# Performance work log

Hardware: AMD Instinct MI355X
Metric: run time of the kernel (lower is better)

## Reference

```python
import jax, jax.numpy as jnp
import numpy as np

DIM = 1024
HIDDEN = 4096
N_EXPERTS = 8
K = 2
TEMP = 1.0


def setup_inputs() -> dict:
    key = jax.random.key(0)
    ks = jax.random.split(key, 7)
    s = 0.02
    x = jax.random.normal(ks[0], (4, 2048, DIM), dtype=jnp.float32)
    router_w = jax.random.normal(ks[1], (N_EXPERTS, DIM), dtype=jnp.float32) * s
    router_b = jnp.zeros((N_EXPERTS,), dtype=jnp.float32)
    # Expert(dim, hidden, 'swiglu'): fc1: dim -> 2*hidden, fc2: hidden -> dim
    w1 = jax.random.normal(ks[2], (N_EXPERTS, 2 * HIDDEN, DIM), dtype=jnp.float32) * s
    b1 = jnp.zeros((N_EXPERTS, 2 * HIDDEN), dtype=jnp.float32)
    w2 = jax.random.normal(ks[3], (N_EXPERTS, DIM, HIDDEN), dtype=jnp.float32) * s
    b2 = jnp.zeros((N_EXPERTS, DIM), dtype=jnp.float32)
    return {"x": x, "router_w": router_w, "router_b": router_b,
            "w1": w1, "b1": b1, "w2": w2, "b2": b2}


def _expert_ffn(xf, wa, ba, wb, bb):
    # xf: [T, dim]; swiglu FFN
    h = xf @ wa.T + ba                       # [T, 2*hidden]
    h1, h2 = jnp.split(h, 2, axis=-1)
    h = jax.nn.silu(h1) * h2                 # [T, hidden]
    return h @ wb.T + bb                     # [T, dim]


def reference(x, router_w, router_b, w1, b1, w2, b2):
    b, t, d = x.shape
    logits = (x @ router_w.T + router_b) / TEMP          # [b, t, E]
    topk_val, topk_idx = jax.lax.top_k(logits, K)        # [b, t, K]
    weights = jax.nn.softmax(topk_val, axis=-1)          # [b, t, K]

    xf = x.reshape(-1, d)                                # [T, dim]
    # Compute every expert on all tokens (dense reference for irregular dispatch)
    outs = jax.vmap(_expert_ffn, in_axes=(None, 0, 0, 0, 0))(xf, w1, b1, w2, b2)  # [E, T, dim]
    outs = jnp.transpose(outs, (1, 0, 2))                # [T, E, dim]

    idx = topk_idx.reshape(-1, K)                        # [T, K]
    gathered = jnp.take_along_axis(outs, idx[:, :, None], axis=1)  # [T, K, dim]
    combined = (gathered * weights.reshape(-1, K, 1)).sum(axis=1)  # [T, dim]
    return combined.reshape(b, t, d)
```

## Files before the change

### kernel.cpp

```cpp
#include <hip/hip_runtime.h>

#define T_TOK 8192
#define DIMX 1024
#define HID 4096
#define NE 8
#define TP (T_TOK * 2)
#define PADR 128
#define BK 64

typedef unsigned short ushort_t;
typedef __attribute__((ext_vector_type(4))) float f32x4;
typedef __attribute__((ext_vector_type(8))) short bf16x8;

__device__ __forceinline__ ushort_t f2bf(float f) {
    unsigned u = __float_as_uint(f);
    u += 0x7FFFu + ((u >> 16) & 1u);
    return (ushort_t)(u >> 16);
}
__device__ __forceinline__ float b2f(ushort_t h) {
    return __uint_as_float(((unsigned)h) << 16);
}

__device__ __forceinline__ void gload_lds16(const void* g, void* l) {
    __builtin_amdgcn_global_load_lds((const __attribute__((address_space(1))) void*)g,
                                     (__attribute__((address_space(3))) void*)l, 16, 0, 0);
}

__device__ __forceinline__ f32x4 mfma16(bf16x8 a, bf16x8 b, f32x4 c) {
    return __builtin_amdgcn_mfma_f32_16x16x32_bf16(a, b, c, 0, 0, 0);
}


__global__ void zero_kernel(int* p) {
    if (threadIdx.x < 16) p[threadIdx.x] = 0;
}

__global__ __launch_bounds__(256) void router_kernel(
    const float* __restrict__ x, const float* __restrict__ rw, const float* __restrict__ rb,
    int* __restrict__ counts, int* __restrict__ topk_idx, float* __restrict__ topk_w)
{
    __shared__ float s_rw[NE * DIMX];
    int tid = threadIdx.x;
    for (int i = tid * 4; i < NE * DIMX; i += 1024) {
        float4 v = *(const float4*)(rw + i);
        *(float4*)(s_rw + i) = v;
    }
    __syncthreads();
    int lane = tid & 63, wid = tid >> 6;
    int t = blockIdx.x * 4 + wid;
    const float* xr = x + (size_t)t * DIMX;
    float acc[NE];
#pragma unroll
    for (int e = 0; e < NE; e++) acc[e] = 0.f;
    for (int j = 0; j < DIMX; j += 64) {
        float xv = xr[j + lane];
#pragma unroll
        for (int e = 0; e < NE; e++) acc[e] += xv * s_rw[e * DIMX + j + lane];
    }
#pragma unroll
    for (int e = 0; e < NE; e++) {
#pragma unroll
        for (int off = 32; off > 0; off >>= 1) acc[e] += __shfl_xor(acc[e], off, 64);
    }
    if (lane == 0) {
        float v[NE];
#pragma unroll
        for (int e = 0; e < NE; e++) v[e] = acc[e] + rb[e];
        int i0 = 0; float b0 = v[0];
#pragma unroll
        for (int e = 1; e < NE; e++) if (v[e] > b0) { b0 = v[e]; i0 = e; }
        int i1 = -1; float b1v = -1e30f;
#pragma unroll
        for (int e = 0; e < NE; e++) if (e != i0 && v[e] > b1v) { b1v = v[e]; i1 = e; }
        float ex = __expf(b1v - b0);
        float inv = 1.f / (1.f + ex);
        topk_idx[t * 2]     = i0;  topk_idx[t * 2 + 1] = i1;
        topk_w[t * 2]       = inv; topk_w[t * 2 + 1]   = ex * inv;
        atomicAdd(&counts[i0], 1); atomicAdd(&counts[i1], 1);
    }
}

__global__ void prefix_kernel(const int* __restrict__ counts, int* __restrict__ offsets) {
    if (threadIdx.x == 0 && blockIdx.x == 0) {
        int s = 0;
        for (int e = 0; e < NE; e++) { offsets[e] = s; s += counts[e]; }
    }
}

__global__ __launch_bounds__(256) void scatter_kernel(
    const int* __restrict__ topk_idx, const float* __restrict__ topk_w,
    const int* __restrict__ offsets, int* __restrict__ cursor,
    int* __restrict__ tok_of, float* __restrict__ w_of, int* __restrict__ slot_of)
{
    int i = blockIdx.x * 256 + threadIdx.x;
    int e = topk_idx[i];
    int pos = offsets[e] + atomicAdd(&cursor[e], 1);
    tok_of[pos] = i >> 1;
    w_of[pos] = topk_w[i];
    slot_of[i] = pos;
}


__global__ __launch_bounds__(256) void cvt_kernel(
    const float* __restrict__ src, ushort_t* __restrict__ dst, int n8)
{
    int i = blockIdx.x * 256 + threadIdx.x;
    if (i >= n8) return;
    float4 a = ((const float4*)src)[i * 2];
    float4 b = ((const float4*)src)[i * 2 + 1];
    ushort4 lo = make_ushort4(f2bf(a.x), f2bf(a.y), f2bf(a.z), f2bf(a.w));
    ushort4 hi = make_ushort4(f2bf(b.x), f2bf(b.y), f2bf(b.z), f2bf(b.w));
    ((ushort4*)dst)[i * 2] = lo;
    ((ushort4*)dst)[i * 2 + 1] = hi;
}

__global__ __launch_bounds__(256) void gather_kernel(
    const float* __restrict__ x, const int* __restrict__ tok_of, ushort_t* __restrict__ Xp)
{
    int pos = blockIdx.x;
    int t = tok_of[pos];
    int i = threadIdx.x;
    float4 v = ((const float4*)(x + (size_t)t * DIMX))[i];
    ushort4 o = make_ushort4(f2bf(v.x), f2bf(v.y), f2bf(v.z), f2bf(v.w));
    ((ushort4*)(Xp + (size_t)pos * DIMX))[i] = o;
}

__global__ __launch_bounds__(256, 2) void fc1_kernel(
    const ushort_t* __restrict__ Xp, const ushort_t* __restrict__ w1b,
    const float* __restrict__ b1,
    const int* __restrict__ counts, const int* __restrict__ offsets,
    ushort_t* __restrict__ H)
{
    const int e = blockIdx.z, mt = blockIdx.y, nt = blockIdx.x;
    const int cnt = counts[e];
    if (mt * 128 >= cnt) return;
    const int base = offsets[e] + mt * 128;
    int rows_valid = cnt - mt * 128; if (rows_valid > 128) rows_valid = 128;

    __shared__ ushort_t As[128 * BK];
    __shared__ ushort_t Bs1[64 * BK];
    __shared__ ushort_t Bs2[64 * BK];

    const int tid = threadIdx.x, lane = tid & 63, wid = tid >> 6;
    const int wave_m = wid >> 1, wave_n = wid & 1;

    const ushort_t* Ag  = Xp + (size_t)base * DIMX;
    const ushort_t* B1g = w1b + ((size_t)e * 2 * HID + (size_t)nt * 64) * DIMX;
    const ushort_t* B2g = B1g + (size_t)HID * DIMX;

    const ushort_t* agp[4]; ushort_t* alp[4];
#pragma unroll
    for (int i = 0; i < 4; i++) {
        int s = wid * 4 + i;
        int r = s * 8 + (lane >> 3);
        int c = (lane & 7) ^ (r & 7);
        agp[i] = Ag + (size_t)r * DIMX + c * 8;
        alp[i] = As + s * 512 + lane * 8;
    }
    const ushort_t* bgp[4]; ushort_t* blp[4];
#pragma unroll
    for (int i = 0; i < 2; i++) {
        int s = wid * 2 + i;
        int r = s * 8 + (lane >> 3);
        int c = (lane & 7) ^ (r & 7);
        bgp[i]     = B1g + (size_t)r * DIMX + c * 8;
        blp[i]     = Bs1 + s * 512 + lane * 8;
        bgp[2 + i] = B2g + (size_t)r * DIMX + c * 8;
        blp[2 + i] = Bs2 + s * 512 + lane * 8;
    }

    f32x4 acc1[4][2], acc2[4][2];
#pragma unroll
    for (int mf = 0; mf < 4; mf++)
#pragma unroll
        for (int nf = 0; nf < 2; nf++) {
            acc1[mf][nf] = (f32x4){0.f, 0.f, 0.f, 0.f};
            acc2[mf][nf] = (f32x4){0.f, 0.f, 0.f, 0.f};
        }

    const int q = lane >> 4, rA = lane & 15;
    for (int ko = 0; ko < DIMX / BK; ko++) {
#pragma unroll
        for (int i = 0; i < 4; i++) gload_lds16(agp[i], alp[i]);
#pragma unroll
        for (int i = 0; i < 4; i++) gload_lds16(bgp[i], blp[i]);
#pragma unroll
        for (int i = 0; i < 4; i++) { agp[i] += BK; bgp[i] += BK; }
        __syncthreads();

        bf16x8 af[4][2], bf1[2][2], bf2[2][2];
#pragma unroll
        for (int mf = 0; mf < 4; mf++) {
            int r = wave_m * 64 + mf * 16 + rA;
            const ushort_t* rp = As + r * BK;
            af[mf][0] = *(const bf16x8*)(rp + ((q    ) ^ (r & 7)) * 8);
            af[mf][1] = *(const bf16x8*)(rp + ((q + 4) ^ (r & 7)) * 8);
        }
#pragma unroll
        for (int nf = 0; nf < 2; nf++) {
            int r = wave_n * 32 + nf * 16 + rA;
            const ushort_t* rp1 = Bs1 + r * BK;
            const ushort_t* rp2 = Bs2 + r * BK;
            bf1[nf][0] = *(const bf16x8*)(rp1 + ((q    ) ^ (r & 7)) * 8);
            bf1[nf][1] = *(const bf16x8*)(rp1 + ((q + 4) ^ (r & 7)) * 8);
            bf2[nf][0] = *(const bf16x8*)(rp2 + ((q    ) ^ (r & 7)) * 8);
            bf2[nf][1] = *(const bf16x8*)(rp2 + ((q + 4) ^ (r & 7)) * 8);
        }
#pragma unroll
        for (int mf = 0; mf < 4; mf++)
#pragma unroll
            for (int nf = 0; nf < 2; nf++) {
                acc1[mf][nf] = mfma16(af[mf][0], bf1[nf][0], acc1[mf][nf]);
                acc1[mf][nf] = mfma16(af[mf][1], bf1[nf][1], acc1[mf][nf]);
                acc2[mf][nf] = mfma16(af[mf][0], bf2[nf][0], acc2[mf][nf]);
                acc2[mf][nf] = mfma16(af[mf][1], bf2[nf][1], acc2[mf][nf]);
            }
        __syncthreads();
    }

    const float* b1p = b1 + (size_t)e * 2 * HID + (size_t)nt * 64;
#pragma unroll
    for (int mf = 0; mf < 4; mf++) {
#pragma unroll
        for (int nf = 0; nf < 2; nf++) {
            int col = wave_n * 32 + nf * 16 + rA;
            float bb1 = b1p[col];
            float bb2 = b1p[HID + col];
#pragma unroll
            for (int rr = 0; rr < 4; rr++) {
                int row = wave_m * 64 + mf * 16 + q * 4 + rr;
                if (row < rows_valid) {
                    float v1 = acc1[mf][nf][rr] + bb1;
                    float v2 = acc2[mf][nf][rr] + bb2;
                    float hv = v1 * v2 / (1.f + __expf(-v1));
                    H[(size_t)(base + row) * HID + (size_t)nt * 64 + col] = f2bf(hv);
                }
            }
        }
    }
}

__global__ __launch_bounds__(256, 2) void fc2_kernel(
    const ushort_t* __restrict__ H, const ushort_t* __restrict__ w2b,
    const float* __restrict__ b2,
    const int* __restrict__ counts, const int* __restrict__ offsets,
    const float* __restrict__ w_of, ushort_t* __restrict__ Os)
{
    const int e = blockIdx.z, mt = blockIdx.x, nt = blockIdx.y;
    const int cnt = counts[e];
    if (mt * 128 >= cnt) return;
    const int base = offsets[e] + mt * 128;
    int rows_valid = cnt - mt * 128; if (rows_valid > 128) rows_valid = 128;

    __shared__ ushort_t As[128 * BK];
    __shared__ ushort_t Bs[128 * BK];

    const int tid = threadIdx.x, lane = tid & 63, wid = tid >> 6;
    const int wave_m = wid >> 1, wave_n = wid & 1;

    const ushort_t* Ag = H + (size_t)base * HID;
    const ushort_t* Bg = w2b + ((size_t)e * DIMX + (size_t)nt * 128) * HID;

    const ushort_t* agp[4]; ushort_t* alp[4];
    const ushort_t* bgp[4]; ushort_t* blp[4];
#pragma unroll
    for (int i = 0; i < 4; i++) {
        int s = wid * 4 + i;
        int r = s * 8 + (lane >> 3);
        int c = (lane & 7) ^ (r & 7);
        agp[i] = Ag + (size_t)r * HID + c * 8;
        alp[i] = As + s * 512 + lane * 8;
        bgp[i] = Bg + (size_t)r * HID + c * 8;
        blp[i] = Bs + s * 512 + lane * 8;
    }

    f32x4 acc[4][4];
#pragma unroll
    for (int mf = 0; mf < 4; mf++)
#pragma unroll
        for (int nf = 0; nf < 4; nf++) acc[mf][nf] = (f32x4){0.f, 0.f, 0.f, 0.f};

    const int q = lane >> 4, rA = lane & 15;
    for (int ko = 0; ko < HID / BK; ko++) {
#pragma unroll
        for (int i = 0; i < 4; i++) gload_lds16(agp[i], alp[i]);
#pragma unroll
        for (int i = 0; i < 4; i++) gload_lds16(bgp[i], blp[i]);
#pragma unroll
        for (int i = 0; i < 4; i++) { agp[i] += BK; bgp[i] += BK; }
        __syncthreads();

        bf16x8 af[4][2], bfr[4][2];
#pragma unroll
        for (int mf = 0; mf < 4; mf++) {
            int r = wave_m * 64 + mf * 16 + rA;
            const ushort_t* rp = As + r * BK;
            af[mf][0] = *(const bf16x8*)(rp + ((q    ) ^ (r & 7)) * 8);
            af[mf][1] = *(const bf16x8*)(rp + ((q + 4) ^ (r & 7)) * 8);
        }
#pragma unroll
        for (int nf = 0; nf < 4; nf++) {
            int r = wave_n * 64 + nf * 16 + rA;
            const ushort_t* rp = Bs + r * BK;
            bfr[nf][0] = *(const bf16x8*)(rp + ((q    ) ^ (r & 7)) * 8);
            bfr[nf][1] = *(const bf16x8*)(rp + ((q + 4) ^ (r & 7)) * 8);
        }
#pragma unroll
        for (int mf = 0; mf < 4; mf++)
#pragma unroll
            for (int nf = 0; nf < 4; nf++) {
                acc[mf][nf] = mfma16(af[mf][0], bfr[nf][0], acc[mf][nf]);
                acc[mf][nf] = mfma16(af[mf][1], bfr[nf][1], acc[mf][nf]);
            }
        __syncthreads();
    }

    const float* b2p = b2 + (size_t)e * DIMX + (size_t)nt * 128;
#pragma unroll
    for (int mf = 0; mf < 4; mf++) {
#pragma unroll
        for (int rr = 0; rr < 4; rr++) {
            int row = wave_m * 64 + mf * 16 + q * 4 + rr;
            if (row < rows_valid) {
                float wv = w_of[base + row];
#pragma unroll
                for (int nf = 0; nf < 4; nf++) {
                    int col = wave_n * 64 + nf * 16 + rA;
                    float val = (acc[mf][nf][rr] + b2p[col]) * wv;
                    Os[(size_t)(base + row) * DIMX + (size_t)nt * 128 + col] = f2bf(val);
                }
            }
        }
    }
}

__global__ __launch_bounds__(256) void combine_kernel(
    const ushort_t* __restrict__ Os, const int* __restrict__ slot_of, float* __restrict__ out)
{
    int t = blockIdx.x;
    int p0 = slot_of[t * 2], p1 = slot_of[t * 2 + 1];
    int i = threadIdx.x;
    ushort4 a = ((const ushort4*)(Os + (size_t)p0 * DIMX))[i];
    ushort4 b = ((const ushort4*)(Os + (size_t)p1 * DIMX))[i];
    float4 o;
    o.x = b2f(a.x) + b2f(b.x);
    o.y = b2f(a.y) + b2f(b.y);
    o.z = b2f(a.z) + b2f(b.z);
    o.w = b2f(a.w) + b2f(b.w);
    ((float4*)(out + (size_t)t * DIMX))[i] = o;
}


extern "C" void kernel_launch(void* const* d_in, const int* in_sizes, int n_in,
                              void* d_out, int out_size, void* d_ws, size_t ws_size,
                              hipStream_t stream) {
    (void)in_sizes; (void)n_in; (void)out_size; (void)ws_size;
    const float* x  = (const float*)d_in[0];
    const float* rw = (const float*)d_in[1];
    const float* rb = (const float*)d_in[2];
    const float* w1 = (const float*)d_in[3];
    const float* b1 = (const float*)d_in[4];
    const float* w2 = (const float*)d_in[5];
    const float* b2 = (const float*)d_in[6];
    float* out = (float*)d_out;

    char* p = (char*)d_ws;
    ushort_t* w1b = (ushort_t*)p; p += (size_t)NE * 2 * HID * DIMX * 2;
    ushort_t* w2b = (ushort_t*)p; p += (size_t)NE * DIMX * HID * 2;
    ushort_t* Xp  = (ushort_t*)p; p += (size_t)(TP + PADR) * DIMX * 2;
    ushort_t* Hb  = (ushort_t*)p; p += (size_t)(TP + PADR) * HID * 2;
    ushort_t* Os  = (ushort_t*)p; p += (size_t)TP * DIMX * 2;
    int* ints     = (int*)p;      p += 24 * sizeof(int);
    int*   counts  = ints;
    int*   cursor  = ints + 8;
    int*   offsets = ints + 16;
    int*   topk_idx = (int*)p;   p += (size_t)TP * 4;
    float* topk_w   = (float*)p; p += (size_t)TP * 4;
    int*   tok_of   = (int*)p;   p += (size_t)TP * 4;
    float* w_of     = (float*)p; p += (size_t)TP * 4;
    int*   slot_of  = (int*)p;   p += (size_t)TP * 4;

    zero_kernel<<<1, 64, 0, stream>>>(counts);
    router_kernel<<<T_TOK / 4, 256, 0, stream>>>(x, rw, rb, counts, topk_idx, topk_w);
    prefix_kernel<<<1, 64, 0, stream>>>(counts, offsets);
    scatter_kernel<<<TP / 256, 256, 0, stream>>>(topk_idx, topk_w, offsets, cursor,
                                                 tok_of, w_of, slot_of);
    cvt_kernel<<<(NE * 2 * HID * DIMX / 8 + 255) / 256, 256, 0, stream>>>(w1, w1b, NE * 2 * HID * DIMX / 8);
    cvt_kernel<<<(NE * DIMX * HID / 8 + 255) / 256, 256, 0, stream>>>(w2, w2b, NE * DIMX * HID / 8);
    gather_kernel<<<TP, 256, 0, stream>>>(x, tok_of, Xp);

    fc1_kernel<<<dim3(HID / 64, 32, NE), 256, 0, stream>>>(Xp, w1b, b1, counts, offsets, Hb);
    fc2_kernel<<<dim3(32, DIMX / 128, NE), 256, 0, stream>>>(Hb, w2b, b2, counts, offsets, w_of, Os);
    combine_kernel<<<T_TOK, 256, 0, stream>>>(Os, slot_of, out);
}
```

Before: 1.356 ms.

## Split fc2 K dimension in two, fold gate weights into combine, merge weight conversions

The fc2 GEMM is split into two halves along the hidden (K) dimension, which doubles the number of blocks. Each half writes bf16 partial sums into buffers reused from Xp and w1b, which are dead after fc1. The routing weight multiply moves from the fc2 epilogue to the combine kernel, which now reads four partial rows per token instead of two. The two weight-conversion launches are merged into one, and the epilogues skip the row bound check for full tiles. In exchange, combine reads more data, and storing the partial sums in bf16 adds rounding error.

```diff
diff --git a/kernel.cpp b/kernel.cpp
--- a/kernel.cpp
+++ b/kernel.cpp
@@ -102,16 +102,22 @@
 
 
 __global__ __launch_bounds__(256) void cvt_kernel(
-    const float* __restrict__ src, ushort_t* __restrict__ dst, int n8)
-{
+    const float* __restrict__ w1, ushort_t* __restrict__ w1d,
+    const float* __restrict__ w2, ushort_t* __restrict__ w2d)
+{
+    const int n8_w1 = NE * 2 * HID * DIMX / 8;
+    const int n8_tot = n8_w1 + NE * DIMX * HID / 8;
     int i = blockIdx.x * 256 + threadIdx.x;
-    if (i >= n8) return;
-    float4 a = ((const float4*)src)[i * 2];
-    float4 b = ((const float4*)src)[i * 2 + 1];
+    if (i >= n8_tot) return;
+    const float* src; ushort_t* dst; int j;
+    if (i < n8_w1) { src = w1; dst = w1d; j = i; }
+    else           { src = w2; dst = w2d; j = i - n8_w1; }
+    float4 a = ((const float4*)src)[j * 2];
+    float4 b = ((const float4*)src)[j * 2 + 1];
     ushort4 lo = make_ushort4(f2bf(a.x), f2bf(a.y), f2bf(a.z), f2bf(a.w));
     ushort4 hi = make_ushort4(f2bf(b.x), f2bf(b.y), f2bf(b.z), f2bf(b.w));
-    ((ushort4*)dst)[i * 2] = lo;
-    ((ushort4*)dst)[i * 2 + 1] = hi;
+    ((ushort4*)dst)[j * 2] = lo;
+    ((ushort4*)dst)[j * 2 + 1] = hi;
 }
 
 __global__ __launch_bounds__(256) void gather_kernel(
@@ -219,6 +225,7 @@
     }
 
     const float* b1p = b1 + (size_t)e * 2 * HID + (size_t)nt * 64;
+    const bool full = (rows_valid == 128);
 #pragma unroll
     for (int mf = 0; mf < 4; mf++) {
 #pragma unroll
@@ -229,7 +236,7 @@
 #pragma unroll
             for (int rr = 0; rr < 4; rr++) {
                 int row = wave_m * 64 + mf * 16 + q * 4 + rr;
-                if (row < rows_valid) {
+                if (full || row < rows_valid) {
                     float v1 = acc1[mf][nf][rr] + bb1;
                     float v2 = acc2[mf][nf][rr] + bb2;
                     float hv = v1 * v2 / (1.f + __expf(-v1));
@@ -244,13 +251,15 @@
     const ushort_t* __restrict__ H, const ushort_t* __restrict__ w2b,
     const float* __restrict__ b2,
     const int* __restrict__ counts, const int* __restrict__ offsets,
-    const float* __restrict__ w_of, ushort_t* __restrict__ Os)
-{
-    const int e = blockIdx.z, mt = blockIdx.x, nt = blockIdx.y;
+    ushort_t* __restrict__ Os0, ushort_t* __restrict__ Os1)
+{
+    const int e = blockIdx.z & 7, kh = blockIdx.z >> 3;
+    const int mt = blockIdx.x, nt = blockIdx.y;
     const int cnt = counts[e];
     if (mt * 128 >= cnt) return;
     const int base = offsets[e] + mt * 128;
     int rows_valid = cnt - mt * 128; if (rows_valid > 128) rows_valid = 128;
+    ushort_t* Os = kh ? Os1 : Os0;
 
     __shared__ ushort_t As[128 * BK];
     __shared__ ushort_t Bs[128 * BK];
@@ -258,8 +267,8 @@
     const int tid = threadIdx.x, lane = tid & 63, wid = tid >> 6;
     const int wave_m = wid >> 1, wave_n = wid & 1;
 
-    const ushort_t* Ag = H + (size_t)base * HID;
-    const ushort_t* Bg = w2b + ((size_t)e * DIMX + (size_t)nt * 128) * HID;
+    const ushort_t* Ag = H + (size_t)base * HID + kh * (HID / 2);
+    const ushort_t* Bg = w2b + ((size_t)e * DIMX + (size_t)nt * 128) * HID + kh * (HID / 2);
 
     const ushort_t* agp[4]; ushort_t* alp[4];
     const ushort_t* bgp[4]; ushort_t* blp[4];
@@ -281,7 +290,7 @@
         for (int nf = 0; nf < 4; nf++) acc[mf][nf] = (f32x4){0.f, 0.f, 0.f, 0.f};
 
     const int q = lane >> 4, rA = lane & 15;
-    for (int ko = 0; ko < HID / BK; ko++) {
+    for (int ko = 0; ko < (HID / 2) / BK; ko++) {
 #pragma unroll
         for (int i = 0; i < 4; i++) gload_lds16(agp[i], alp[i]);
 #pragma unroll
@@ -316,17 +325,18 @@
     }
 
     const float* b2p = b2 + (size_t)e * DIMX + (size_t)nt * 128;
+    const float bscale = (kh == 0) ? 1.f : 0.f;
+    const bool full = (rows_valid == 128);
 #pragma unroll
     for (int mf = 0; mf < 4; mf++) {
 #pragma unroll
         for (int rr = 0; rr < 4; rr++) {
             int row = wave_m * 64 + mf * 16 + q * 4 + rr;
-            if (row < rows_valid) {
-                float wv = w_of[base + row];
+            if (full || row < rows_valid) {
 #pragma unroll
                 for (int nf = 0; nf < 4; nf++) {
                     int col = wave_n * 64 + nf * 16 + rA;
-                    float val = (acc[mf][nf][rr] + b2p[col]) * wv;
+                    float val = acc[mf][nf][rr] + b2p[col] * bscale;
                     Os[(size_t)(base + row) * DIMX + (size_t)nt * 128 + col] = f2bf(val);
                 }
             }
@@ -335,18 +345,22 @@
 }
 
 __global__ __launch_bounds__(256) void combine_kernel(
-    const ushort_t* __restrict__ Os, const int* __restrict__ slot_of, float* __restrict__ out)
+    const ushort_t* __restrict__ Os0, const ushort_t* __restrict__ Os1,
+    const int* __restrict__ slot_of, const float* __restrict__ w_of, float* __restrict__ out)
 {
     int t = blockIdx.x;
     int p0 = slot_of[t * 2], p1 = slot_of[t * 2 + 1];
+    float w0 = w_of[p0], w1 = w_of[p1];
     int i = threadIdx.x;
-    ushort4 a = ((const ushort4*)(Os + (size_t)p0 * DIMX))[i];
-    ushort4 b = ((const ushort4*)(Os + (size_t)p1 * DIMX))[i];
+    ushort4 a0 = ((const ushort4*)(Os0 + (size_t)p0 * DIMX))[i];
+    ushort4 a1 = ((const ushort4*)(Os1 + (size_t)p0 * DIMX))[i];
+    ushort4 b0 = ((const ushort4*)(Os0 + (size_t)p1 * DIMX))[i];
+    ushort4 b1 = ((const ushort4*)(Os1 + (size_t)p1 * DIMX))[i];
     float4 o;
-    o.x = b2f(a.x) + b2f(b.x);
-    o.y = b2f(a.y) + b2f(b.y);
-    o.z = b2f(a.z) + b2f(b.z);
-    o.w = b2f(a.w) + b2f(b.w);
+    o.x = w0 * (b2f(a0.x) + b2f(a1.x)) + w1 * (b2f(b0.x) + b2f(b1.x));
+    o.y = w0 * (b2f(a0.y) + b2f(a1.y)) + w1 * (b2f(b0.y) + b2f(b1.y));
+    o.z = w0 * (b2f(a0.z) + b2f(a1.z)) + w1 * (b2f(b0.z) + b2f(b1.z));
+    o.w = w0 * (b2f(a0.w) + b2f(a1.w)) + w1 * (b2f(b0.w) + b2f(b1.w));
     ((float4*)(out + (size_t)t * DIMX))[i] = o;
 }
 
@@ -369,7 +383,6 @@
     ushort_t* w2b = (ushort_t*)p; p += (size_t)NE * DIMX * HID * 2;
     ushort_t* Xp  = (ushort_t*)p; p += (size_t)(TP + PADR) * DIMX * 2;
     ushort_t* Hb  = (ushort_t*)p; p += (size_t)(TP + PADR) * HID * 2;
-    ushort_t* Os  = (ushort_t*)p; p += (size_t)TP * DIMX * 2;
     int* ints     = (int*)p;      p += 24 * sizeof(int);
     int*   counts  = ints;
     int*   cursor  = ints + 8;
@@ -379,17 +392,21 @@
     int*   tok_of   = (int*)p;   p += (size_t)TP * 4;
     float* w_of     = (float*)p; p += (size_t)TP * 4;
     int*   slot_of  = (int*)p;   p += (size_t)TP * 4;
+    ushort_t* Os0 = Xp;
+    ushort_t* Os1 = w1b;
 
     zero_kernel<<<1, 64, 0, stream>>>(counts);
     router_kernel<<<T_TOK / 4, 256, 0, stream>>>(x, rw, rb, counts, topk_idx, topk_w);
     prefix_kernel<<<1, 64, 0, stream>>>(counts, offsets);
     scatter_kernel<<<TP / 256, 256, 0, stream>>>(topk_idx, topk_w, offsets, cursor,
                                                  tok_of, w_of, slot_of);
-    cvt_kernel<<<(NE * 2 * HID * DIMX / 8 + 255) / 256, 256, 0, stream>>>(w1, w1b, NE * 2 * HID * DIMX / 8);
-    cvt_kernel<<<(NE * DIMX * HID / 8 + 255) / 256, 256, 0, stream>>>(w2, w2b, NE * DIMX * HID / 8);
+    {
+        int n8_tot = NE * 2 * HID * DIMX / 8 + NE * DIMX * HID / 8;
+        cvt_kernel<<<(n8_tot + 255) / 256, 256, 0, stream>>>(w1, w1b, w2, w2b);
+    }
     gather_kernel<<<TP, 256, 0, stream>>>(x, tok_of, Xp);
 
     fc1_kernel<<<dim3(HID / 64, 32, NE), 256, 0, stream>>>(Xp, w1b, b1, counts, offsets, Hb);
-    fc2_kernel<<<dim3(32, DIMX / 128, NE), 256, 0, stream>>>(Hb, w2b, b2, counts, offsets, w_of, Os);
-    combine_kernel<<<T_TOK, 256, 0, stream>>>(Os, slot_of, out);
-}
+    fc2_kernel<<<dim3(32, DIMX / 128, NE * 2), 256, 0, stream>>>(Hb, w2b, b2, counts, offsets, Os0, Os1);
+    combine_kernel<<<T_TOK, 256, 0, stream>>>(Os0, Os1, slot_of, w_of, out);
+}
```

New measurement: 1.371 ms. About the same (+1.1%).
